# Optimization experiments

Hardware: AMD Instinct MI355X
Metric: run time of the kernel (lower is better)

Reference implementation:

```python
import jax, jax.numpy as jnp
import numpy as np

B, H, S_PAST, S_NEW, D = 4, 32, 4096, 16, 128


def setup_inputs() -> dict:
    key = jax.random.key(0)
    k1, k2, k3, k4 = jax.random.split(key, 4)
    return {
        "past_key": jax.random.normal(k1, (B, H, S_PAST, D), dtype=jnp.float32),
        "past_value": jax.random.normal(k2, (B, H, S_PAST, D), dtype=jnp.float32),
        "key_states": jax.random.normal(k3, (B, H, S_NEW, D), dtype=jnp.float32),
        "value_states": jax.random.normal(k4, (B, H, S_NEW, D), dtype=jnp.float32),
    }


def reference(past_key, past_value, key_states, value_states):
    # DynamicCache.update: append new tokens along the sequence axis (dim=-2)
    k = jnp.concatenate([past_key, key_states], axis=-2)   # [B,H,S_past+S_new,D]
    v = jnp.concatenate([past_value, value_states], axis=-2)
    return (k, v)
```

## Files before the change

### kernel.cpp

```cpp
#include <hip/hip_runtime.h>


typedef float f4 __attribute__((ext_vector_type(4)));

constexpr unsigned B = 4, H = 32, S_PAST = 4096, S_NEW = 16, D = 128;
constexpr unsigned ROW4   = D / 4;
constexpr unsigned S_TOT  = S_PAST + S_NEW;
constexpr unsigned CHUNK4 = S_TOT * ROW4;
constexpr unsigned HALF4  = B * H * CHUNK4;
constexpr unsigned PASTC4 = S_PAST * ROW4;
constexpr unsigned NEWC4  = S_NEW * ROW4;
constexpr unsigned PAST_TOTAL4 = 2u * B * H * PASTC4;
constexpr unsigned PAST_BLOCKS = 2048;
constexpr unsigned SEG4 = PAST_TOTAL4 / PAST_BLOCKS;
constexpr unsigned NEW_BLOCKS = 2u * B * H;

__global__ __launch_bounds__(256) void dyncache_copy_kernel(
    const f4* __restrict__ pk, const f4* __restrict__ pv,
    const f4* __restrict__ nk, const f4* __restrict__ nv,
    f4* __restrict__ out)
{
    const unsigned tid = threadIdx.x;
    if (blockIdx.x < PAST_BLOCKS) {
        const unsigned seg = blockIdx.x * SEG4;
        const unsigned t   = seg >> 24;
        const unsigned loc = seg & ((1u << 24) - 1);
        const unsigned bh  = loc >> 17;
        const unsigned off = loc & (PASTC4 - 1);
        const f4* __restrict__ src =
            (t ? pv : pk) + ((size_t)bh << 17) + off;
        f4* __restrict__ dst =
            out + (size_t)t * HALF4 + (size_t)bh * CHUNK4 + off;
        #pragma unroll 8
        for (unsigned k = 0; k < SEG4 / 256u; ++k) {
            const unsigned i = k * 256u + tid;
            __builtin_nontemporal_store(__builtin_nontemporal_load(src + i), dst + i);
        }
    } else {
        const unsigned blk = blockIdx.x - PAST_BLOCKS;
        const unsigned t   = blk >> 7;
        const unsigned bh  = blk & (B * H - 1);
        const f4* __restrict__ src = (t ? nv : nk) + (size_t)bh * NEWC4;
        f4* __restrict__ dst =
            out + (size_t)t * HALF4 + (size_t)bh * CHUNK4 + PASTC4;
        #pragma unroll
        for (unsigned k = 0; k < NEWC4 / 256u; ++k) {
            const unsigned i = k * 256u + tid;
            __builtin_nontemporal_store(__builtin_nontemporal_load(src + i), dst + i);
        }
    }
}

extern "C" void kernel_launch(void* const* d_in, const int* in_sizes, int n_in,
                              void* d_out, int out_size, void* d_ws, size_t ws_size,
                              hipStream_t stream) {
    const f4* pk = (const f4*)d_in[0];
    const f4* pv = (const f4*)d_in[1];
    const f4* nk = (const f4*)d_in[2];
    const f4* nv = (const f4*)d_in[3];
    f4* out = (f4*)d_out;

    dyncache_copy_kernel<<<PAST_BLOCKS + NEW_BLOCKS, 256, 0, stream>>>(
        pk, pv, nk, nv, out);
}
```

Measured before the change: 211.3 us.

## Software-pipeline the cache copy with register double buffers and fewer blocks

Halves the grid to 1024 blocks and has each thread double-buffer groups of 12 vector loads in registers, overlapping loads of the next group with stores of the previous one. The new-token append is folded into the first 256 blocks instead of separate blocks. The aim is more outstanding memory requests per thread to get closer to HBM bandwidth. The cost is higher register use, a coarser grid, and slight imbalance for the blocks that also do the append.

```diff
diff --git a/kernel.cpp b/kernel.cpp
--- a/kernel.cpp
+++ b/kernel.cpp
@@ -11,44 +11,81 @@
 constexpr unsigned PASTC4 = S_PAST * ROW4;
 constexpr unsigned NEWC4  = S_NEW * ROW4;
 constexpr unsigned PAST_TOTAL4 = 2u * B * H * PASTC4;
-constexpr unsigned PAST_BLOCKS = 2048;
-constexpr unsigned SEG4 = PAST_TOTAL4 / PAST_BLOCKS;
-constexpr unsigned NEW_BLOCKS = 2u * B * H;
+constexpr unsigned BLOCKS = 1024;
+constexpr unsigned SEG4  = PAST_TOTAL4 / BLOCKS;
+constexpr unsigned ITERS = SEG4 / 256u;
+constexpr unsigned GRP   = 12;
+constexpr unsigned NGRP  = ITERS / GRP;
+constexpr unsigned REM   = ITERS - NGRP * GRP;
 
-__global__ __launch_bounds__(256) void dyncache_copy_kernel(
+__global__ __launch_bounds__(256, 4) void dyncache_copy_kernel(
     const f4* __restrict__ pk, const f4* __restrict__ pv,
     const f4* __restrict__ nk, const f4* __restrict__ nv,
     f4* __restrict__ out)
 {
     const unsigned tid = threadIdx.x;
-    if (blockIdx.x < PAST_BLOCKS) {
-        const unsigned seg = blockIdx.x * SEG4;
-        const unsigned t   = seg >> 24;
-        const unsigned loc = seg & ((1u << 24) - 1);
-        const unsigned bh  = loc >> 17;
-        const unsigned off = loc & (PASTC4 - 1);
-        const f4* __restrict__ src =
-            (t ? pv : pk) + ((size_t)bh << 17) + off;
-        f4* __restrict__ dst =
-            out + (size_t)t * HALF4 + (size_t)bh * CHUNK4 + off;
-        #pragma unroll 8
-        for (unsigned k = 0; k < SEG4 / 256u; ++k) {
-            const unsigned i = k * 256u + tid;
-            __builtin_nontemporal_store(__builtin_nontemporal_load(src + i), dst + i);
-        }
-    } else {
-        const unsigned blk = blockIdx.x - PAST_BLOCKS;
-        const unsigned t   = blk >> 7;
-        const unsigned bh  = blk & (B * H - 1);
-        const f4* __restrict__ src = (t ? nv : nk) + (size_t)bh * NEWC4;
-        f4* __restrict__ dst =
+
+    if (blockIdx.x < 2u * B * H) {
+        const unsigned t  = blockIdx.x >> 7;
+        const unsigned bh = blockIdx.x & (B * H - 1);
+        const f4* __restrict__ s = (t ? nv : nk) + (size_t)bh * NEWC4;
+        f4* __restrict__ d =
             out + (size_t)t * HALF4 + (size_t)bh * CHUNK4 + PASTC4;
         #pragma unroll
-        for (unsigned k = 0; k < NEWC4 / 256u; ++k) {
-            const unsigned i = k * 256u + tid;
-            __builtin_nontemporal_store(__builtin_nontemporal_load(src + i), dst + i);
-        }
+        for (unsigned k = 0; k < NEWC4 / 256u; ++k)
+            __builtin_nontemporal_store(
+                __builtin_nontemporal_load(s + k * 256u + tid), d + k * 256u + tid);
     }
+
+    const unsigned seg = blockIdx.x * SEG4;
+    const unsigned t   = seg >> 24;
+    const unsigned loc = seg & ((1u << 24) - 1);
+    const unsigned bh  = loc >> 17;
+    const unsigned off = loc & (PASTC4 - 1);
+    const f4* __restrict__ src =
+        (t ? pv : pk) + ((size_t)bh << 17) + off + tid;
+    f4* __restrict__ dst =
+        out + (size_t)t * HALF4 + (size_t)bh * CHUNK4 + off + tid;
+
+    f4 a[GRP], b[GRP];
+
+    #pragma unroll
+    for (unsigned j = 0; j < GRP; ++j)
+        a[j] = __builtin_nontemporal_load(src + (0u * GRP + j) * 256u);
+
+    #pragma unroll
+    for (unsigned p = 0; p < 4; ++p) {
+        const unsigned g1 = 2u * p + 1u;
+        #pragma unroll
+        for (unsigned j = 0; j < GRP; ++j)
+            b[j] = __builtin_nontemporal_load(src + (g1 * GRP + j) * 256u);
+        #pragma unroll
+        for (unsigned j = 0; j < GRP; ++j)
+            __builtin_nontemporal_store(a[j], dst + ((g1 - 1u) * GRP + j) * 256u);
+        const unsigned g2 = 2u * p + 2u;
+        #pragma unroll
+        for (unsigned j = 0; j < GRP; ++j)
+            a[j] = __builtin_nontemporal_load(src + (g2 * GRP + j) * 256u);
+        #pragma unroll
+        for (unsigned j = 0; j < GRP; ++j)
+            __builtin_nontemporal_store(b[j], dst + ((g2 - 1u) * GRP + j) * 256u);
+    }
+    #pragma unroll
+    for (unsigned j = 0; j < GRP; ++j)
+        b[j] = __builtin_nontemporal_load(src + (9u * GRP + j) * 256u);
+    #pragma unroll
+    for (unsigned j = 0; j < GRP; ++j)
+        __builtin_nontemporal_store(a[j], dst + (8u * GRP + j) * 256u);
+    #pragma unroll
+    for (unsigned j = 0; j < GRP; ++j)
+        __builtin_nontemporal_store(b[j], dst + (9u * GRP + j) * 256u);
+
+    #pragma unroll
+    for (unsigned j = 0; j < REM; ++j)
+        a[j] = __builtin_nontemporal_load(src + (NGRP * GRP + j) * 256u);
+    #pragma unroll
+    for (unsigned j = 0; j < REM; ++j)
+        __builtin_nontemporal_store(a[j], dst + (NGRP * GRP + j) * 256u);
 }
 
 extern "C" void kernel_launch(void* const* d_in, const int* in_sizes, int n_in,
@@ -60,6 +97,5 @@
     const f4* nv = (const f4*)d_in[3];
     f4* out = (f4*)d_out;
 
-    dyncache_copy_kernel<<<PAST_BLOCKS + NEW_BLOCKS, 256, 0, stream>>>(
-        pk, pv, nk, nv, out);
+    dyncache_copy_kernel<<<BLOCKS, 256, 0, stream>>>(pk, pv, nk, nv, out);
 }
```

After: 190.5 us. -9.8%, faster.
